# Kernel optimization log

Hardware: AMD Instinct MI355X
Metric: run time of the kernel (lower is better)

Reference implementation:

```python
import jax, jax.numpy as jnp
import numpy as np

B, C, H, W = 64, 512, 28, 28
K = 52  # ceil(0.1 * 512)


def setup_inputs() -> dict:
    key = jax.random.key(0)
    x = jax.random.normal(key, (B, C, H, W), dtype=jnp.float32)
    return {"x": x, "k": K}


def reference(x, k):
    # ---- hard k-winners plasticity mask (affects gradients only) ----
    xt = jnp.moveaxis(x, 1, -1)                      # [B, H, W, C]
    _, idx = jax.lax.top_k(xt, k)                    # [B, H, W, k] indices into C
    mask_t = jnp.put_along_axis(
        jnp.zeros(xt.shape, dtype=jnp.bool_), idx, True, axis=-1, inplace=False
    )
    mask = jnp.moveaxis(mask_t, -1, 1)               # [B, C, H, W]
    # where(mask, x, stop_grad(x)) -- forward value is just x
    plastic = jnp.where(mask, x, jax.lax.stop_gradient(x))
    # ---- soft competition: subtract per-position channel mean, ReLU ----
    means = jax.lax.stop_gradient(jnp.mean(plastic, axis=1, keepdims=True))  # [B,1,H,W]
    return jax.nn.relu(plastic - means)
```

## Files before the change

### kernel.cpp

```cpp
#include <hip/hip_runtime.h>


#define B_DIM 64
#define C_DIM 512
#define HW4   196
#define TX    16
#define TY    16
#define CPT   (C_DIM / TY)
#define NW    4

typedef __attribute__((ext_vector_type(4))) float f4;

__global__ __launch_bounds__(256, 3) void kwinners_fwd(const float* __restrict__ x,
                                                       float* __restrict__ out) {
    __shared__ f4 part[NW][TX];

    const int tid = threadIdx.x;
    const int tx  = tid & (TX - 1);
    const int ty  = tid >> 4;
    const int w   = tid >> 6;

    const int g   = blockIdx.x * TX + tx;
    const int b   = g / HW4;
    const int hw4 = g - b * HW4;

    const f4* __restrict__ xb =
        reinterpret_cast<const f4*>(x) + (size_t)b * C_DIM * HW4 + hw4;
    f4* __restrict__ ob =
        reinterpret_cast<f4*>(out) + (size_t)b * C_DIM * HW4 + hw4;

    const int c0 = ty * CPT;

    f4 v[CPT];
    #pragma unroll
    for (int cc = 0; cc < CPT; ++cc) {
        v[cc] = xb[(c0 + cc) * HW4];
    }

    f4 s = (f4)(0.0f);
    #pragma unroll
    for (int cc = 0; cc < CPT; ++cc) s += v[cc];

    #pragma unroll
    for (int m = 16; m <= 32; m <<= 1) {
        s.x += __shfl_xor(s.x, m);
        s.y += __shfl_xor(s.y, m);
        s.z += __shfl_xor(s.z, m);
        s.w += __shfl_xor(s.w, m);
    }

    if ((tid & 63) < TX) part[w][tx] = s;
    __syncthreads();

    f4 m4 = (f4)(0.0f);
    #pragma unroll
    for (int ww = 0; ww < NW; ++ww) m4 += part[ww][tx];
    m4 *= (1.0f / (float)C_DIM);

    #pragma unroll
    for (int cc = 0; cc < CPT; ++cc) {
        f4 r = v[cc] - m4;
        r.x = fmaxf(r.x, 0.f);
        r.y = fmaxf(r.y, 0.f);
        r.z = fmaxf(r.z, 0.f);
        r.w = fmaxf(r.w, 0.f);
        __builtin_nontemporal_store(r, &ob[(cc + c0) * HW4]);
    }
}

extern "C" void kernel_launch(void* const* d_in, const int* in_sizes, int n_in,
                              void* d_out, int out_size, void* d_ws, size_t ws_size,
                              hipStream_t stream) {
    const float* x  = (const float*)d_in[0];
    float* out = (float*)d_out;

    const int groups = B_DIM * HW4;
    dim3 grid(groups / TX);
    dim3 block(256);
    hipLaunchKernelGGL(kwinners_fwd, grid, block, 0, stream, x, out);
}
```

Before: 40.63 us.

## Stream channel sums and re-read input instead of caching values in registers

Replaces the register-resident per-thread channel slice with a two-pass scheme: each wavefront sums 32 channels for 64 consecutive positions, reduces through shared memory, then re-reads the input to apply the mean subtraction and ReLU. Blocks grow to 1024 threads covering 64 positions, widening contiguous accesses and cutting register pressure. In exchange it reads the input twice, relying on cache hits for the second pass, and the grid shrinks to fewer blocks than compute units.

```diff
diff --git a/kernel.cpp b/kernel.cpp
--- a/kernel.cpp
+++ b/kernel.cpp
@@ -4,67 +4,50 @@
 #define B_DIM 64
 #define C_DIM 512
 #define HW4   196
-#define TX    16
-#define TY    16
-#define CPT   (C_DIM / TY)
-#define NW    4
+#define TILE  64
+#define NW    16
+#define CPW   (C_DIM / NW)
 
 typedef __attribute__((ext_vector_type(4))) float f4;
 
-__global__ __launch_bounds__(256, 3) void kwinners_fwd(const float* __restrict__ x,
-                                                       float* __restrict__ out) {
-    __shared__ f4 part[NW][TX];
+__global__ __launch_bounds__(1024) void kwinners_fwd(const float* __restrict__ x,
+                                                     float* __restrict__ out) {
+    __shared__ f4 part[NW][TILE];
 
-    const int tid = threadIdx.x;
-    const int tx  = tid & (TX - 1);
-    const int ty  = tid >> 4;
-    const int w   = tid >> 6;
+    const int tid  = threadIdx.x;
+    const int lane = tid & 63;
+    const int wv   = tid >> 6;
 
-    const int g   = blockIdx.x * TX + tx;
+    const int g   = blockIdx.x * TILE + lane;
     const int b   = g / HW4;
     const int hw4 = g - b * HW4;
 
-    const f4* __restrict__ xb =
-        reinterpret_cast<const f4*>(x) + (size_t)b * C_DIM * HW4 + hw4;
-    f4* __restrict__ ob =
-        reinterpret_cast<f4*>(out) + (size_t)b * C_DIM * HW4 + hw4;
-
-    const int c0 = ty * CPT;
-
-    f4 v[CPT];
-    #pragma unroll
-    for (int cc = 0; cc < CPT; ++cc) {
-        v[cc] = xb[(c0 + cc) * HW4];
-    }
+    const size_t base = (size_t)b * C_DIM * HW4 + (size_t)(wv * CPW) * HW4 + hw4;
+    const f4* __restrict__ xp = reinterpret_cast<const f4*>(x) + base;
+    f4* __restrict__ op       = reinterpret_cast<f4*>(out) + base;
 
     f4 s = (f4)(0.0f);
-    #pragma unroll
-    for (int cc = 0; cc < CPT; ++cc) s += v[cc];
+    #pragma unroll 8
+    for (int cc = 0; cc < CPW; ++cc)
+        s += xp[(size_t)cc * HW4];
 
-    #pragma unroll
-    for (int m = 16; m <= 32; m <<= 1) {
-        s.x += __shfl_xor(s.x, m);
-        s.y += __shfl_xor(s.y, m);
-        s.z += __shfl_xor(s.z, m);
-        s.w += __shfl_xor(s.w, m);
-    }
-
-    if ((tid & 63) < TX) part[w][tx] = s;
+    part[wv][lane] = s;
     __syncthreads();
 
-    f4 m4 = (f4)(0.0f);
+    f4 m = (f4)(0.0f);
     #pragma unroll
-    for (int ww = 0; ww < NW; ++ww) m4 += part[ww][tx];
-    m4 *= (1.0f / (float)C_DIM);
+    for (int ww = 0; ww < NW; ++ww) m += part[ww][lane];
+    m *= (1.0f / (float)C_DIM);
 
-    #pragma unroll
-    for (int cc = 0; cc < CPT; ++cc) {
-        f4 r = v[cc] - m4;
+    #pragma unroll 8
+    for (int cc = 0; cc < CPW; ++cc) {
+        f4 v = xp[(size_t)cc * HW4];
+        f4 r = v - m;
         r.x = fmaxf(r.x, 0.f);
         r.y = fmaxf(r.y, 0.f);
         r.z = fmaxf(r.z, 0.f);
         r.w = fmaxf(r.w, 0.f);
-        __builtin_nontemporal_store(r, &ob[(cc + c0) * HW4]);
+        __builtin_nontemporal_store(r, &op[(size_t)cc * HW4]);
     }
 }
 
@@ -75,7 +58,7 @@
     float* out = (float*)d_out;
 
     const int groups = B_DIM * HW4;
-    dim3 grid(groups / TX);
-    dim3 block(256);
+    dim3 grid(groups / TILE);
+    dim3 block(1024);
     hipLaunchKernelGGL(kwinners_fwd, grid, block, 0, stream, x, out);
 }
```

Measured after the change: 51.53 us. 1.27x slower.
